# Kernel optimization log

Hardware: AMD Instinct MI355X
Metric: run time of the kernel (lower is better)

## Reference

```python
import jax, jax.numpy as jnp
import numpy as np

N, E, S = 20000, 160000, 3        # nodes, edges, message-passing steps
L, NODE_D, EDGE_D, OUT = 128, 12, 7, 3
LN_EPS = 1e-5


def _mlp(x, W0, b0, W1, b1, W2, b2):
    # Linear -> ReLU -> Linear -> ReLU -> Linear (widths: in->L->L->out)
    h = jax.nn.relu(x @ W0 + b0)
    h = jax.nn.relu(h @ W1 + b1)
    return h @ W2 + b2


def _ln(h, g, b):
    mu = jnp.mean(h, axis=-1, keepdims=True)
    var = jnp.mean((h - mu) ** 2, axis=-1, keepdims=True)
    return (h - mu) * jax.lax.rsqrt(var + LN_EPS) * g + b


def setup_inputs() -> dict:
    ks = iter(jax.random.split(jax.random.key(0), 64))
    w = lambda *s: jax.random.normal(next(ks), s, jnp.float32) * 0.05
    z = lambda *s: jnp.zeros(s, jnp.float32)
    o = lambda *s: jnp.ones(s, jnp.float32)
    inp = {
        'node_x': jax.random.normal(next(ks), (N, NODE_D), jnp.float32),
        'edge_x': jax.random.normal(next(ks), (E, EDGE_D), jnp.float32),
        'enc_n_W0': w(NODE_D, L), 'enc_n_b0': z(L), 'enc_n_W1': w(L, L), 'enc_n_b1': z(L),
        'enc_n_W2': w(L, L), 'enc_n_b2': z(L), 'enc_n_g': o(L), 'enc_n_be': z(L),
        'enc_e_W0': w(EDGE_D, L), 'enc_e_b0': z(L), 'enc_e_W1': w(L, L), 'enc_e_b1': z(L),
        'enc_e_W2': w(L, L), 'enc_e_b2': z(L), 'enc_e_g': o(L), 'enc_e_be': z(L),
        'gnb_e_W0': w(S, 3 * L, L), 'gnb_e_b0': z(S, L), 'gnb_e_W1': w(S, L, L), 'gnb_e_b1': z(S, L),
        'gnb_e_W2': w(S, L, L), 'gnb_e_b2': z(S, L), 'gnb_e_g': o(S, L), 'gnb_e_be': z(S, L),
        'gnb_n_W0': w(S, 2 * L, L), 'gnb_n_b0': z(S, L), 'gnb_n_W1': w(S, L, L), 'gnb_n_b1': z(S, L),
        'gnb_n_W2': w(S, L, L), 'gnb_n_b2': z(S, L), 'gnb_n_g': o(S, L), 'gnb_n_be': z(S, L),
        'dec_W0': w(L, L), 'dec_b0': z(L), 'dec_W1': w(L, L), 'dec_b1': z(L),
        'dec_W2': w(L, OUT), 'dec_b2': z(OUT),
        'senders': jax.random.randint(next(ks), (E,), 0, N, jnp.int32),
        'receivers': jax.random.randint(next(ks), (E,), 0, N, jnp.int32),
    }
    return inp


def reference(node_x, edge_x,
              enc_n_W0, enc_n_b0, enc_n_W1, enc_n_b1, enc_n_W2, enc_n_b2, enc_n_g, enc_n_be,
              enc_e_W0, enc_e_b0, enc_e_W1, enc_e_b1, enc_e_W2, enc_e_b2, enc_e_g, enc_e_be,
              gnb_e_W0, gnb_e_b0, gnb_e_W1, gnb_e_b1, gnb_e_W2, gnb_e_b2, gnb_e_g, gnb_e_be,
              gnb_n_W0, gnb_n_b0, gnb_n_W1, gnb_n_b1, gnb_n_W2, gnb_n_b2, gnb_n_g, gnb_n_be,
              dec_W0, dec_b0, dec_W1, dec_b1, dec_W2, dec_b2,
              senders, receivers):
    num_nodes = node_x.shape[0]
    # Encoder: MLP + LayerNorm on nodes and edges
    nf = _ln(_mlp(node_x, enc_n_W0, enc_n_b0, enc_n_W1, enc_n_b1, enc_n_W2, enc_n_b2), enc_n_g, enc_n_be)
    ef = _ln(_mlp(edge_x, enc_e_W0, enc_e_b0, enc_e_W1, enc_e_b1, enc_e_W2, enc_e_b2), enc_e_g, enc_e_be)

    def step(carry, p):
        nf, ef = carry
        (eW0, eb0, eW1, eb1, eW2, eb2, eg, ebe,
         nW0, nb0, nW1, nb1, nW2, nb2, ng, nbe) = p
        # gather sender/receiver node features -> concat with edge features -> edge MLP
        cat_e = jnp.concatenate([nf[senders], nf[receivers], ef], axis=-1)  # [E, 3L]
        new_ef = _ln(_mlp(cat_e, eW0, eb0, eW1, eb1, eW2, eb2), eg, ebe)
        # scatter-sum updated edge features to receiver nodes
        agg = jax.ops.segment_sum(new_ef, receivers, num_segments=num_nodes)  # [N, L]
        new_nf = _ln(_mlp(jnp.concatenate([nf, agg], axis=-1), nW0, nb0, nW1, nb1, nW2, nb2), ng, nbe)
        # residual connections on both nodes and edges
        return (nf + new_nf, ef + new_ef), None

    step_params = (gnb_e_W0, gnb_e_b0, gnb_e_W1, gnb_e_b1, gnb_e_W2, gnb_e_b2, gnb_e_g, gnb_e_be,
                   gnb_n_W0, gnb_n_b0, gnb_n_W1, gnb_n_b1, gnb_n_W2, gnb_n_b2, gnb_n_g, gnb_n_be)
    (nf, ef), _ = jax.lax.scan(step, (nf, ef), step_params)

    # Decoder: MLP without LayerNorm
    return _mlp(nf, dec_W0, dec_b0, dec_W1, dec_b1, dec_W2, dec_b2)
```

## Files before the change

kernel.cpp:

```cpp
#include <hip/hip_runtime.h>
#include <hip/hip_bf16.h>

#define NN 20000
#define EE 160000

typedef __attribute__((ext_vector_type(8))) short bf16x8;
typedef __attribute__((ext_vector_type(4))) float f32x4;

__device__ __forceinline__ unsigned short f2bf(float f) {
    unsigned int u = __float_as_uint(f);
    u += 0x7FFFu + ((u >> 16) & 1);
    return (unsigned short)(u >> 16);
}
__device__ __forceinline__ float bf2f(short s) {
    return __uint_as_float(((unsigned int)(unsigned short)s) << 16);
}
__device__ __forceinline__ bf16x8 pack8(float4 a, float4 b) {
    bf16x8 r;
    r[0] = (short)f2bf(a.x); r[1] = (short)f2bf(a.y);
    r[2] = (short)f2bf(a.z); r[3] = (short)f2bf(a.w);
    r[4] = (short)f2bf(b.x); r[5] = (short)f2bf(b.y);
    r[6] = (short)f2bf(b.z); r[7] = (short)f2bf(b.w);
    return r;
}

#define SH_STRIDE 136
#define SW_STRIDE 56
#define SH64 132
#define SW64 72

__device__ __forceinline__ void bar_lgkm() {
    asm volatile("s_waitcnt lgkmcnt(0)\n\ts_barrier" ::: "memory");
}

__device__ __forceinline__ void mfma_sweep_lds(f32x4 (&acc)[2][8], bf16x8 a0, bf16x8 a1,
                                               const short* sWb, int lm, int lq)
{
#pragma unroll
    for (int ct = 0; ct < 8; ++ct) {
        bf16x8 b = *(const bf16x8*)(sWb + (ct * 16 + lm) * SW_STRIDE + lq * 8);
        acc[0][ct] = __builtin_amdgcn_mfma_f32_16x16x32_bf16(a0, b, acc[0][ct], 0, 0, 0);
        acc[1][ct] = __builtin_amdgcn_mfma_f32_16x16x32_bf16(a1, b, acc[1][ct], 0, 0, 0);
    }
}

__device__ __forceinline__ void mfma_sweep64(f32x4 (&acc)[2][8], bf16x8 a0, bf16x8 a1,
                                             const short* sWb, int colOff, int lm)
{
#pragma unroll
    for (int ct = 0; ct < 8; ++ct) {
        bf16x8 b = *(const bf16x8*)(sWb + (ct * 16 + lm) * SW64 + colOff);
        acc[0][ct] = __builtin_amdgcn_mfma_f32_16x16x32_bf16(a0, b, acc[0][ct], 0, 0, 0);
        acc[1][ct] = __builtin_amdgcn_mfma_f32_16x16x32_bf16(a1, b, acc[1][ct], 0, 0, 0);
    }
}

template<int NT>
struct WStage { bf16x8 v[512 / NT]; };

template<int NT>
__device__ __forceinline__ void wload(WStage<NT>& ws, const short* __restrict__ Wt,
                                      int Kpad, int k0, int tid)
{
#pragma unroll
    for (int j = 0; j < 256 / NT; ++j) {
        int i = tid + j * NT;
        int r = i >> 1, h = i & 1;
        const short* src = Wt + (size_t)r * Kpad + k0 + h * 16;
        ws.v[2 * j]     = *(const bf16x8*)src;
        ws.v[2 * j + 1] = *(const bf16x8*)(src + 8);
    }
}
template<int NT>
__device__ __forceinline__ void wstore(const WStage<NT>& ws, short* __restrict__ sW, int tid)
{
#pragma unroll
    for (int j = 0; j < 256 / NT; ++j) {
        int i = tid + j * NT;
        int r = i >> 1, h = i & 1;
        short* dst = sW + r * SW_STRIDE + h * 16;
        *(bf16x8*)dst       = ws.v[2 * j];
        *(bf16x8*)(dst + 8) = ws.v[2 * j + 1];
    }
}

struct WStage64 { bf16x8 v[4]; };
__device__ __forceinline__ void wload64(WStage64& ws, const short* __restrict__ Wt,
                                        int Kpad, int k0, int tid)
{
#pragma unroll
    for (int j = 0; j < 4; ++j) {
        int i = tid + j * 256;
        int r = i >> 3, h = i & 7;
        ws.v[j] = *(const bf16x8*)(Wt + (size_t)r * Kpad + k0 + h * 8);
    }
}
__device__ __forceinline__ void wstore64(const WStage64& ws, short* __restrict__ sW, int tid)
{
#pragma unroll
    for (int j = 0; j < 4; ++j) {
        int i = tid + j * 256;
        int r = i >> 3, h = i & 7;
        *(bf16x8*)(sW + r * SW64 + h * 8) = ws.v[j];
    }
}

__device__ __forceinline__ void zero_acc(f32x4 (&acc)[2][8]) {
#pragma unroll
    for (int i = 0; i < 2; ++i)
#pragma unroll
        for (int j = 0; j < 8; ++j) acc[i][j] = (f32x4)(0.f);
}

__device__ __forceinline__ void park(const f32x4 (&acc)[2][8], const float* __restrict__ bias,
                                     short* __restrict__ sH, int w32, int lm, int lq)
{
#pragma unroll
    for (int ct = 0; ct < 8; ++ct) {
        float bb = bias[ct * 16 + lm];
#pragma unroll
        for (int rt = 0; rt < 2; ++rt) {
            int rbase = w32 + rt * 16 + lq * 4;
#pragma unroll
            for (int reg = 0; reg < 4; ++reg) {
                float v = fmaxf(acc[rt][ct][reg] + bb, 0.f);
                sH[(rbase + reg) * SH_STRIDE + ct * 16 + lm] = (short)f2bf(v);
            }
        }
    }
}

__device__ __forceinline__ void park64(const f32x4 (&acc)[2][8], const float* __restrict__ bias,
                                       short* __restrict__ sH, int w32, int lm, int lq)
{
#pragma unroll
    for (int ct = 0; ct < 8; ++ct) {
        float bb = bias[ct * 16 + lm];
#pragma unroll
        for (int rt = 0; rt < 2; ++rt) {
            int rbase = w32 + rt * 16 + lq * 4;
#pragma unroll
            for (int reg = 0; reg < 4; ++reg) {
                float v = fmaxf(acc[rt][ct][reg] + bb, 0.f);
                sH[(rbase + reg) * SH64 + ct * 16 + lm] = (short)f2bf(v);
            }
        }
    }
}

struct Frag {
    bf16x8 a0, a1;
    float4 f0, f1, f2, f3;
    int isF;
};

template<int MODE>
__device__ __forceinline__ void load_frag(Frag& fr, int c,
    const short* __restrict__ nfb, const float* __restrict__ aggf,
    int r0m, int r1m, const short* sH, int w32, int lm, int lq)
{
    int kq = lq * 8;
    fr.isF = 0;
    if (MODE == 0) {
        fr.a0 = *(const bf16x8*)&sH[(w32 + lm) * SH_STRIDE + c * 32 + kq];
        fr.a1 = *(const bf16x8*)&sH[(w32 + 16 + lm) * SH_STRIDE + c * 32 + kq];
    } else if (MODE == 2) {
        int seg = c >> 2, kb = (c & 3) * 32 + kq;
        if (seg == 0) {
            fr.a0 = *(const bf16x8*)(nfb + (size_t)r0m * 128 + kb);
            fr.a1 = *(const bf16x8*)(nfb + (size_t)r1m * 128 + kb);
        } else {
            const float* p0 = aggf + (size_t)r0m * 128 + kb;
            const float* p1 = aggf + (size_t)r1m * 128 + kb;
            fr.f0 = *(const float4*)p0; fr.f1 = *(const float4*)(p0 + 4);
            fr.f2 = *(const float4*)p1; fr.f3 = *(const float4*)(p1 + 4);
            fr.isF = 1;
        }
    } else {
        int kb = c * 32 + kq;
        fr.a0 = *(const bf16x8*)(nfb + (size_t)r0m * 128 + kb);
        fr.a1 = *(const bf16x8*)(nfb + (size_t)r1m * 128 + kb);
    }
}

struct Frag64 { bf16x8 a[4]; };

__device__ __forceinline__ void load_frag64(Frag64& fr, int c,
    const short* __restrict__ nfb, const short* __restrict__ efHi,
    int iS0, int iS1, int iR0, int iR1, size_t eO0, size_t eO1, int lq)
{
    int kb = (c & 1) * 64 + lq * 8;
    int seg = c >> 1;
    const short *base0, *base1;
    if (seg == 0)      { base0 = nfb + (size_t)iS0 * 128; base1 = nfb + (size_t)iS1 * 128; }
    else if (seg == 1) { base0 = nfb + (size_t)iR0 * 128; base1 = nfb + (size_t)iR1 * 128; }
    else               { base0 = efHi + eO0;              base1 = efHi + eO1; }
    fr.a[0] = *(const bf16x8*)(base0 + kb);
    fr.a[1] = *(const bf16x8*)(base1 + kb);
    fr.a[2] = *(const bf16x8*)(base0 + kb + 32);
    fr.a[3] = *(const bf16x8*)(base1 + kb + 32);
}

template<int RESID>
__global__ __launch_bounds__(256) void gnn_edge64(
    const short* __restrict__ Wt0,
    const short* __restrict__ Wt1, const short* __restrict__ Wt2,
    const float* __restrict__ b0, const float* __restrict__ b1, const float* __restrict__ b2,
    const float* __restrict__ g, const float* __restrict__ be,
    const short* __restrict__ nfb,
    short* __restrict__ efHi, short* __restrict__ efLo,
    const int* __restrict__ eList,
    const int* __restrict__ senders, const int* __restrict__ receivers,
    float* __restrict__ aggOut)
{
    __shared__ short sH[128 * SH64];
    __shared__ short sW[128 * SW64];
    __shared__ int sRcv[128], sSnd[128];
    const int tid = threadIdx.x;
    const int lane = tid & 63;
    const int w = tid >> 6;
    const int lm = lane & 15;
    const int lq = lane >> 4;
    const int w32 = w * 32;
    const int m0 = blockIdx.x * 128;

    if (tid < 128) {
        int slot = m0 + tid;
        int e = eList ? eList[slot] : slot;
        sRcv[tid] = receivers[e];
        sSnd[tid] = senders[e];
    }
    bar_lgkm();

    f32x4 acc[2][8];
    zero_acc(acc);

    const int s0 = w32 + 2 * lm, s1 = s0 + 1;
    const int iS0 = sSnd[s0], iS1 = sSnd[s1];
    const int iR0 = sRcv[s0], iR1 = sRcv[s1];
    const size_t eO0 = (size_t)(m0 + s0) * 128;
    const size_t eO1 = (size_t)(m0 + s1) * 128;

    {
        WStage64 ws, wsn;
        Frag64 cur, nxt;
        wload64(ws, Wt0, 384, 0, tid);
        load_frag64(cur, 0, nfb, efHi, iS0, iS1, iR0, iR1, eO0, eO1, lq);
#pragma unroll
        for (int c = 0; c < 6; ++c) {
            if (c + 1 < 6) {
                wload64(wsn, Wt0, 384, (c + 1) * 64, tid);
                load_frag64(nxt, c + 1, nfb, efHi, iS0, iS1, iR0, iR1, eO0, eO1, lq);
            }
            bar_lgkm();
            wstore64(ws, sW, tid);
            bar_lgkm();
            mfma_sweep64(acc, cur.a[0], cur.a[1], sW, lq * 8, lm);
            mfma_sweep64(acc, cur.a[2], cur.a[3], sW, 32 + lq * 8, lm);
            ws = wsn; cur = nxt;
        }
    }
    bar_lgkm();
    park64(acc, b0, sH, w32, lm, lq);

    zero_acc(acc);
    {
        WStage64 ws, wsn;
        wload64(ws, Wt1, 128, 0, tid);
#pragma unroll
        for (int c = 0; c < 2; ++c) {
            if (c == 0) wload64(wsn, Wt1, 128, 64, tid);
            bf16x8 a0h0 = *(const bf16x8*)&sH[(w32 + lm) * SH64 + c * 64 + lq * 8];
            bf16x8 a1h0 = *(const bf16x8*)&sH[(w32 + 16 + lm) * SH64 + c * 64 + lq * 8];
            bf16x8 a0h1 = *(const bf16x8*)&sH[(w32 + lm) * SH64 + c * 64 + 32 + lq * 8];
            bf16x8 a1h1 = *(const bf16x8*)&sH[(w32 + 16 + lm) * SH64 + c * 64 + 32 + lq * 8];
            bar_lgkm();
            wstore64(ws, sW, tid);
            bar_lgkm();
            mfma_sweep64(acc, a0h0, a1h0, sW, lq * 8, lm);
            mfma_sweep64(acc, a0h1, a1h1, sW, 32 + lq * 8, lm);
            ws = wsn;
        }
    }
    bar_lgkm();
    park64(acc, b1, sH, w32, lm, lq);

    zero_acc(acc);
    {
        WStage64 ws, wsn;
        wload64(ws, Wt2, 128, 0, tid);
#pragma unroll
        for (int c = 0; c < 2; ++c) {
            if (c == 0) wload64(wsn, Wt2, 128, 64, tid);
            bf16x8 a0h0 = *(const bf16x8*)&sH[(w32 + lm) * SH64 + c * 64 + lq * 8];
            bf16x8 a1h0 = *(const bf16x8*)&sH[(w32 + 16 + lm) * SH64 + c * 64 + lq * 8];
            bf16x8 a0h1 = *(const bf16x8*)&sH[(w32 + lm) * SH64 + c * 64 + 32 + lq * 8];
            bf16x8 a1h1 = *(const bf16x8*)&sH[(w32 + 16 + lm) * SH64 + c * 64 + 32 + lq * 8];
            bar_lgkm();
            wstore64(ws, sW, tid);
            bar_lgkm();
            mfma_sweep64(acc, a0h0, a1h0, sW, lq * 8, lm);
            mfma_sweep64(acc, a0h1, a1h1, sW, 32 + lq * 8, lm);
            ws = wsn;
        }
    }

    float g_[8], be_[8], b2_[8];
#pragma unroll
    for (int ct = 0; ct < 8; ++ct) {
        g_[ct] = g[ct * 16 + lm]; be_[ct] = be[ct * 16 + lm]; b2_[ct] = b2[ct * 16 + lm];
    }
    float run[8];
    int curRcv = -1;
#pragma unroll
    for (int j = 0; j < 8; ++j) {
        int rt = j & 1, reg = j >> 1;
        int rloc = w32 + lq * 8 + j;
        float v[8];
        float s = 0.f;
#pragma unroll
        for (int ct = 0; ct < 8; ++ct) { v[ct] = acc[rt][ct][reg] + b2_[ct]; s += v[ct]; }
        s += __shfl_xor(s, 1); s += __shfl_xor(s, 2);
        s += __shfl_xor(s, 4); s += __shfl_xor(s, 8);
        float mu = s * (1.f / 128.f);
        float q = 0.f;
#pragma unroll
        for (int ct = 0; ct < 8; ++ct) { v[ct] -= mu; q += v[ct] * v[ct]; }
        q += __shfl_xor(q, 1); q += __shfl_xor(q, 2);
        q += __shfl_xor(q, 4); q += __shfl_xor(q, 8);
        float rs = rsqrtf(q * (1.f / 128.f) + 1e-5f);
        int rcv = sRcv[rloc];
        float o[8];
#pragma unroll
        for (int ct = 0; ct < 8; ++ct) {
            o[ct] = v[ct] * rs * g_[ct] + be_[ct];
            if (RESID) {
                size_t gi = (size_t)(m0 + rloc) * 128 + ct * 16 + lm;
                float x = bf2f(efHi[gi]) + bf2f(efLo[gi]) + o[ct];
                short h = (short)f2bf(x);
                efHi[gi] = h;
                efLo[gi] = (short)f2bf(x - bf2f(h));
            }
        }
        if (rcv != curRcv) {
            if (curRcv >= 0) {
#pragma unroll
                for (int ct = 0; ct < 8; ++ct)
                    atomicAdd(aggOut + (size_t)curRcv * 128 + ct * 16 + lm, run[ct]);
            }
            curRcv = rcv;
#pragma unroll
            for (int ct = 0; ct < 8; ++ct) run[ct] = o[ct];
        } else {
#pragma unroll
            for (int ct = 0; ct < 8; ++ct) run[ct] += o[ct];
        }
    }
    if (curRcv >= 0) {
#pragma unroll
        for (int ct = 0; ct < 8; ++ct)
            atomicAdd(aggOut + (size_t)curRcv * 128 + ct * 16 + lm, run[ct]);
    }
}

template<int NW, int MODE, int PAIR>
__global__ __launch_bounds__(NW * 64) void gnn_mlp(
    const short* __restrict__ Wt0,
    const short* __restrict__ Wt1, const short* __restrict__ Wt2,
    const float* __restrict__ b0, const float* __restrict__ b1, const float* __restrict__ b2,
    const float* __restrict__ g, const float* __restrict__ be,
    const float* __restrict__ A0f, int K0,
    const short* __restrict__ nfb,
    const float* __restrict__ aggf,
    const int* __restrict__ eList,
    float* __restrict__ outF, short* __restrict__ outB, short* __restrict__ outB2,
    float* __restrict__ aggOut,
    float* __restrict__ decOut,
    int M, int resid)
{
    constexpr int KP0 = (MODE == 2) ? 256 : (MODE == 3) ? 128 : 32;
    constexpr int nC0 = KP0 / 32;
    __shared__ short sH[NW * 32 * SH_STRIDE];
    __shared__ short sW[128 * SW_STRIDE];
    const int tid = threadIdx.x;
    const int lane = tid & 63;
    const int w = tid >> 6;
    const int lm = lane & 15;
    const int lq = lane >> 4;
    const int w32 = w * 32;
    const int m0 = blockIdx.x * (NW * 32);
    constexpr int NT = NW * 64;

    f32x4 acc[2][8];
    zero_acc(acc);

    if (MODE == 0) {
#pragma unroll
        for (int i = 0; i < 16; ++i) {
            int flat = lane + i * 64;
            int r = flat >> 5, k = flat & 31;
            int row = m0 + w32 + r;
            float v = 0.f;
            if (k < K0 && row < M) {
                int src = eList ? eList[row] : row;
                v = A0f[(size_t)src * K0 + k];
            }
            sH[(w32 + r) * SH_STRIDE + k] = (short)f2bf(v);
        }
    }
    const int r0m = min(m0 + w32 + lm, M - 1);
    const int r1m = min(m0 + w32 + 16 + lm, M - 1);

    {
        WStage<NT> ws, wsn;
        Frag cur, nx1, nx2;
        wload<NT>(ws, Wt0, KP0, 0, tid);
        load_frag<MODE>(cur, 0, nfb, aggf, r0m, r1m, sH, w32, lm, lq);
        if (nC0 > 1)
            load_frag<MODE>(nx1, 1, nfb, aggf, r0m, r1m, sH, w32, lm, lq);
#pragma unroll
        for (int c = 0; c < nC0; ++c) {
            if (c + 1 < nC0)
                wload<NT>(wsn, Wt0, KP0, (c + 1) * 32, tid);
            if (c + 2 < nC0)
                load_frag<MODE>(nx2, c + 2, nfb, aggf, r0m, r1m, sH, w32, lm, lq);
            bar_lgkm();
            wstore<NT>(ws, sW, tid);
            bar_lgkm();
            bf16x8 u0, u1;
            if (cur.isF) { u0 = pack8(cur.f0, cur.f1); u1 = pack8(cur.f2, cur.f3); }
            else         { u0 = cur.a0;               u1 = cur.a1; }
            mfma_sweep_lds(acc, u0, u1, sW, lm, lq);
            ws = wsn; cur = nx1; nx1 = nx2;
        }
    }
    bar_lgkm();
    park(acc, b0, sH, w32, lm, lq);

    if (MODE == 2 && aggOut) {
        int totalF4 = NW * 32 * 32;
        for (int i = tid; i < totalF4; i += NT) {
            int r = i >> 5, c4 = i & 31;
            int row = m0 + r;
            if (row < M)
                *(float4*)(aggOut + (size_t)row * 128 + c4 * 4) = make_float4(0.f, 0.f, 0.f, 0.f);
        }
    }

    zero_acc(acc);
    {
        WStage<NT> ws, wsn;
        wload<NT>(ws, Wt1, 128, 0, tid);
#pragma unroll
        for (int c = 0; c < 4; ++c) {
            if (c + 1 < 4) wload<NT>(wsn, Wt1, 128, (c + 1) * 32, tid);
            bf16x8 a0 = *(const bf16x8*)&sH[(w32 + lm) * SH_STRIDE + c * 32 + lq * 8];
            bf16x8 a1 = *(const bf16x8*)&sH[(w32 + 16 + lm) * SH_STRIDE + c * 32 + lq * 8];
            bar_lgkm();
            wstore<NT>(ws, sW, tid);
            bar_lgkm();
            mfma_sweep_lds(acc, a0, a1, sW, lm, lq);
            ws = wsn;
        }
    }
    bar_lgkm();
    park(acc, b1, sH, w32, lm, lq);

    if (MODE == 3) {
#pragma unroll
        for (int t = 0; t < 2; ++t) {
            int idx = t * 64 + lane;
            if (idx < 96) {
                int r = idx / 3, o = idx - r * 3;
                int row = m0 + w32 + r;
                if (row < M) {
                    float s = b2[o];
#pragma unroll
                    for (int kk = 0; kk < 16; ++kk) {
                        bf16x8 h8 = *(const bf16x8*)&sH[(w32 + r) * SH_STRIDE + kk * 8];
#pragma unroll
                        for (int j = 0; j < 8; ++j)
                            s += bf2f(h8[j]) * A0f[(kk * 8 + j) * 3 + o];
                    }
                    decOut[(size_t)row * 3 + o] = s;
                }
            }
        }
        return;
    }

    zero_acc(acc);
    {
        WStage<NT> ws, wsn;
        wload<NT>(ws, Wt2, 128, 0, tid);
#pragma unroll
        for (int c = 0; c < 4; ++c) {
            if (c + 1 < 4) wload<NT>(wsn, Wt2, 128, (c + 1) * 32, tid);
            bf16x8 a0 = *(const bf16x8*)&sH[(w32 + lm) * SH_STRIDE + c * 32 + lq * 8];
            bf16x8 a1 = *(const bf16x8*)&sH[(w32 + 16 + lm) * SH_STRIDE + c * 32 + lq * 8];
            bar_lgkm();
            wstore<NT>(ws, sW, tid);
            bar_lgkm();
            mfma_sweep_lds(acc, a0, a1, sW, lm, lq);
            ws = wsn;
        }
    }

    float g_[8], be_[8], b2_[8];
#pragma unroll
    for (int ct = 0; ct < 8; ++ct) {
        g_[ct] = g[ct * 16 + lm]; be_[ct] = be[ct * 16 + lm]; b2_[ct] = b2[ct * 16 + lm];
    }
#pragma unroll
    for (int rt = 0; rt < 2; ++rt) {
#pragma unroll
        for (int reg = 0; reg < 4; ++reg) {
            int row = m0 + w32 + rt * 16 + lq * 4 + reg;
            float v[8];
            float s = 0.f;
#pragma unroll
            for (int ct = 0; ct < 8; ++ct) { v[ct] = acc[rt][ct][reg] + b2_[ct]; s += v[ct]; }
            s += __shfl_xor(s, 1); s += __shfl_xor(s, 2);
            s += __shfl_xor(s, 4); s += __shfl_xor(s, 8);
            float mu = s * (1.f / 128.f);
            float q = 0.f;
#pragma unroll
            for (int ct = 0; ct < 8; ++ct) { v[ct] -= mu; q += v[ct] * v[ct]; }
            q += __shfl_xor(q, 1); q += __shfl_xor(q, 2);
            q += __shfl_xor(q, 4); q += __shfl_xor(q, 8);
            float rs = rsqrtf(q * (1.f / 128.f) + 1e-5f);
            if (row < M) {
#pragma unroll
                for (int ct = 0; ct < 8; ++ct) {
                    float o = v[ct] * rs * g_[ct] + be_[ct];
                    size_t gi = (size_t)row * 128 + ct * 16 + lm;
                    if (PAIR) {
                        short h = (short)f2bf(o);
                        outB[gi]  = h;
                        outB2[gi] = (short)f2bf(o - bf2f(h));
                    } else {
                        if (resid) {
                            float ns = outF[gi] + o;
                            outF[gi] = ns;
                            if (outB) outB[gi] = (short)f2bf(ns);
                        } else {
                            outF[gi] = o;
                            if (outB) outB[gi] = (short)f2bf(o);
                        }
                    }
                }
            }
        }
    }
}

__global__ void zero_i(int* __restrict__ p, int n)
{
    int i = blockIdx.x * 256 + threadIdx.x;
    if (i < n) p[i] = 0;
}
__global__ void csr_count(const int* __restrict__ recv, int* __restrict__ cnt, int E)
{
    int i = blockIdx.x * 256 + threadIdx.x;
    if (i < E) atomicAdd(&cnt[recv[i]], 1);
}
__global__ __launch_bounds__(256) void csr_scan(const int* __restrict__ cnt,
                                                int* __restrict__ cursor, int N)
{
    __shared__ int ssum[257];
    const int tid = threadIdx.x;
    const int per = (N + 255) / 256;
    const int lo = tid * per, hi = min(lo + per, N);
    int s = 0;
    for (int i = lo; i < hi; ++i) s += cnt[i];
    ssum[tid] = s;
    __syncthreads();
    if (tid == 0) {
        int run = 0;
        for (int i = 0; i < 256; ++i) { int t = ssum[i]; ssum[i] = run; run += t; }
        ssum[256] = run;
    }
    __syncthreads();
    int run = ssum[tid];
    for (int i = lo; i < hi; ++i) { int c = cnt[i]; cursor[i] = run; run += c; }
}
__global__ void csr_fill(const int* __restrict__ recv, int* __restrict__ cursor,
                         int* __restrict__ eList, int E)
{
    int i = blockIdx.x * 256 + threadIdx.x;
    if (i < E) {
        int pos = atomicAdd(&cursor[recv[i]], 1);
        eList[pos] = i;
    }
}

struct WtPrep { const float* src; int K; int Kpad; int dstOff; };
struct WtPrepAll { WtPrep m[26]; };

__global__ void wt_prep_kernel(WtPrepAll all, short* __restrict__ dst)
{
    const WtPrep p = all.m[blockIdx.y];
    int total = 128 * p.Kpad;
    int idx = blockIdx.x * 256 + threadIdx.x;
    if (idx >= total) return;
    int n = idx / p.Kpad, k = idx - n * p.Kpad;
    float v = (k < p.K) ? p.src[(size_t)k * 128 + n] : 0.f;
    dst[p.dstOff + idx] = (short)f2bf(v);
}

__global__ void zero_kernel(float4* __restrict__ p, long n4)
{
    long i = (long)blockIdx.x * blockDim.x + threadIdx.x;
    if (i < n4) p[i] = make_float4(0.f, 0.f, 0.f, 0.f);
}

extern "C" void kernel_launch(void* const* d_in, const int* in_sizes, int n_in,
                              void* d_out, int out_size, void* d_ws, size_t ws_size,
                              hipStream_t stream)
{
    const float* node_x   = (const float*)d_in[0];
    const float* edge_x   = (const float*)d_in[1];
    const float* enc_n_W0 = (const float*)d_in[2];
    const float* enc_n_b0 = (const float*)d_in[3];
    const float* enc_n_W1 = (const float*)d_in[4];
    const float* enc_n_b1 = (const float*)d_in[5];
    const float* enc_n_W2 = (const float*)d_in[6];
    const float* enc_n_b2 = (const float*)d_in[7];
    const float* enc_n_g  = (const float*)d_in[8];
    const float* enc_n_be = (const float*)d_in[9];
    const float* enc_e_W0 = (const float*)d_in[10];
    const float* enc_e_b0 = (const float*)d_in[11];
    const float* enc_e_W1 = (const float*)d_in[12];
    const float* enc_e_b1 = (const float*)d_in[13];
    const float* enc_e_W2 = (const float*)d_in[14];
    const float* enc_e_b2 = (const float*)d_in[15];
    const float* enc_e_g  = (const float*)d_in[16];
    const float* enc_e_be = (const float*)d_in[17];
    const float* gnb_e_W0 = (const float*)d_in[18];
    const float* gnb_e_b0 = (const float*)d_in[19];
    const float* gnb_e_W1 = (const float*)d_in[20];
    const float* gnb_e_b1 = (const float*)d_in[21];
    const float* gnb_e_W2 = (const float*)d_in[22];
    const float* gnb_e_b2 = (const float*)d_in[23];
    const float* gnb_e_g  = (const float*)d_in[24];
    const float* gnb_e_be = (const float*)d_in[25];
    const float* gnb_n_W0 = (const float*)d_in[26];
    const float* gnb_n_b0 = (const float*)d_in[27];
    const float* gnb_n_W1 = (const float*)d_in[28];
    const float* gnb_n_b1 = (const float*)d_in[29];
    const float* gnb_n_W2 = (const float*)d_in[30];
    const float* gnb_n_b2 = (const float*)d_in[31];
    const float* gnb_n_g  = (const float*)d_in[32];
    const float* gnb_n_be = (const float*)d_in[33];
    const float* dec_W0   = (const float*)d_in[34];
    const float* dec_b0   = (const float*)d_in[35];
    const float* dec_W1   = (const float*)d_in[36];
    const float* dec_b1   = (const float*)d_in[37];
    const float* dec_W2   = (const float*)d_in[38];
    const float* dec_b2   = (const float*)d_in[39];
    const int*   senders  = (const int*)d_in[40];
    const int*   receivers= (const int*)d_in[41];
    float* out = (float*)d_out;

    const int N = NN, E = EE;
    const int WT_TOTAL = (32 + 128 + 128 + 32 + 128 + 128 + 3 * (384 + 128 + 128 + 256 + 128 + 128)
                          + 128 + 128) * 128;

    float* nf   = (float*)d_ws;
    float* agg  = nf + (size_t)N * 128;
    short* efHi = (short*)(agg + (size_t)N * 128);
    short* efLo = efHi + (size_t)E * 128;
    short* nfbf = efLo + (size_t)E * 128;
    short* wt   = nfbf + (size_t)N * 128;
    int*   eList = (int*)(wt + WT_TOTAL);
    size_t need_sorted = (size_t)((char*)(eList + E) - (char*)d_ws);
    int* cnt    = (int*)agg;
    int* cursor = cnt + N;

    const bool useSorted = (ws_size >= need_sorted);
    const int* eL = useSorted ? eList : nullptr;

    WtPrepAll tbl;
    int nMat = 0, off = 0;
    int o_encn[3], o_ence[3], o_ge0[3], o_ge1[3], o_ge2[3], o_gn0[3], o_gn1[3], o_gn2[3], o_dec[2];
    auto add = [&](const float* src, int K, int Kpad) {
        tbl.m[nMat].src = src; tbl.m[nMat].K = K; tbl.m[nMat].Kpad = Kpad;
        tbl.m[nMat].dstOff = off;
        int r = off; off += 128 * Kpad; ++nMat; return r;
    };
    o_encn[0] = add(enc_n_W0, 12, 32);
    o_encn[1] = add(enc_n_W1, 128, 128);
    o_encn[2] = add(enc_n_W2, 128, 128);
    o_ence[0] = add(enc_e_W0, 7, 32);
    o_ence[1] = add(enc_e_W1, 128, 128);
    o_ence[2] = add(enc_e_W2, 128, 128);
    for (int s = 0; s < 3; ++s) {
        o_ge0[s] = add(gnb_e_W0 + (size_t)s * 384 * 128, 384, 384);
        o_ge1[s] = add(gnb_e_W1 + (size_t)s * 128 * 128, 128, 128);
        o_ge2[s] = add(gnb_e_W2 + (size_t)s * 128 * 128, 128, 128);
        o_gn0[s] = add(gnb_n_W0 + (size_t)s * 256 * 128, 256, 256);
        o_gn1[s] = add(gnb_n_W1 + (size_t)s * 128 * 128, 128, 128);
        o_gn2[s] = add(gnb_n_W2 + (size_t)s * 128 * 128, 128, 128);
    }
    o_dec[0] = add(dec_W0, 128, 128);
    o_dec[1] = add(dec_W1, 128, 128);

    wt_prep_kernel<<<dim3(192, 26), 256, 0, stream>>>(tbl, wt);

    if (useSorted) {
        zero_i<<<dim3((N + 255) / 256), 256, 0, stream>>>(cnt, N);
        csr_count<<<dim3((E + 255) / 256), 256, 0, stream>>>(receivers, cnt, E);
        csr_scan<<<dim3(1), 256, 0, stream>>>(cnt, cursor, N);
        csr_fill<<<dim3((E + 255) / 256), 256, 0, stream>>>(receivers, cursor, eList, E);
    }
    zero_kernel<<<dim3((N * 32 + 255) / 256), 256, 0, stream>>>((float4*)agg, (long)N * 32);

    const dim3 gE(E / 128);
    const dim3 gN2((N + 63) / 64);

    gnn_mlp<2, 0, 0><<<gN2, 128, 0, stream>>>(wt + o_encn[0], wt + o_encn[1], wt + o_encn[2],
        enc_n_b0, enc_n_b1, enc_n_b2, enc_n_g, enc_n_be,
        node_x, 12, nullptr, nullptr, nullptr,
        nf, nfbf, nullptr, nullptr, nullptr, N, 0);
    gnn_mlp<4, 0, 1><<<gE, 256, 0, stream>>>(wt + o_ence[0], wt + o_ence[1], wt + o_ence[2],
        enc_e_b0, enc_e_b1, enc_e_b2, enc_e_g, enc_e_be,
        edge_x, 7, nullptr, nullptr, eL,
        nullptr, efHi, efLo, nullptr, nullptr, E, 0);

    for (int s = 0; s < 3; ++s) {
        const float* eb0 = gnb_e_b0 + (size_t)s * 128;
        const float* eb1 = gnb_e_b1 + (size_t)s * 128;
        const float* eb2 = gnb_e_b2 + (size_t)s * 128;
        const float* eg  = gnb_e_g  + (size_t)s * 128;
        const float* ebe = gnb_e_be + (size_t)s * 128;
        const float* nb0 = gnb_n_b0 + (size_t)s * 128;
        const float* nb1 = gnb_n_b1 + (size_t)s * 128;
        const float* nb2 = gnb_n_b2 + (size_t)s * 128;
        const float* ng  = gnb_n_g  + (size_t)s * 128;
        const float* nbe = gnb_n_be + (size_t)s * 128;

        if (s < 2) {
            gnn_edge64<1><<<gE, 256, 0, stream>>>(wt + o_ge0[s], wt + o_ge1[s], wt + o_ge2[s],
                eb0, eb1, eb2, eg, ebe,
                nfbf, efHi, efLo, eL, senders, receivers, agg);
        } else {
            gnn_edge64<0><<<gE, 256, 0, stream>>>(wt + o_ge0[s], wt + o_ge1[s], wt + o_ge2[s],
                eb0, eb1, eb2, eg, ebe,
                nfbf, efHi, efLo, eL, senders, receivers, agg);
        }
        gnn_mlp<2, 2, 0><<<gN2, 128, 0, stream>>>(wt + o_gn0[s], wt + o_gn1[s], wt + o_gn2[s],
            nb0, nb1, nb2, ng, nbe,
            nullptr, 0, nfbf, agg, nullptr,
            nf, nfbf, nullptr, agg, nullptr, N, 1);
    }

    gnn_mlp<2, 3, 0><<<gN2, 128, 0, stream>>>(wt + o_dec[0], wt + o_dec[1], nullptr,
        dec_b0, dec_b1, dec_b2, nullptr, nullptr,
        dec_W2, 0, nfbf, nullptr, nullptr,
        nullptr, nullptr, nullptr, nullptr, out, N, 0);
}
```

Measured before the change: 608.7 us.

## Read MFMA weight fragments directly from global memory instead of LDS staging

```diff
diff --git a/kernel.cpp b/kernel.cpp
--- a/kernel.cpp
+++ b/kernel.cpp
@@ -25,83 +25,17 @@
 }
 
 #define SH_STRIDE 136
-#define SW_STRIDE 56
 #define SH64 132
-#define SW64 72
-
-__device__ __forceinline__ void bar_lgkm() {
-    asm volatile("s_waitcnt lgkmcnt(0)\n\ts_barrier" ::: "memory");
-}
-
-__device__ __forceinline__ void mfma_sweep_lds(f32x4 (&acc)[2][8], bf16x8 a0, bf16x8 a1,
-                                               const short* sWb, int lm, int lq)
+
+template<int KPAD>
+__device__ __forceinline__ void mfma_sweepG(f32x4 (&acc)[2][8], bf16x8 a0, bf16x8 a1,
+                                            const short* __restrict__ Bp)
 {
 #pragma unroll
     for (int ct = 0; ct < 8; ++ct) {
-        bf16x8 b = *(const bf16x8*)(sWb + (ct * 16 + lm) * SW_STRIDE + lq * 8);
+        bf16x8 b = *(const bf16x8*)(Bp + (size_t)ct * 16 * KPAD);
         acc[0][ct] = __builtin_amdgcn_mfma_f32_16x16x32_bf16(a0, b, acc[0][ct], 0, 0, 0);
         acc[1][ct] = __builtin_amdgcn_mfma_f32_16x16x32_bf16(a1, b, acc[1][ct], 0, 0, 0);
-    }
-}
-
-__device__ __forceinline__ void mfma_sweep64(f32x4 (&acc)[2][8], bf16x8 a0, bf16x8 a1,
-                                             const short* sWb, int colOff, int lm)
-{
-#pragma unroll
-    for (int ct = 0; ct < 8; ++ct) {
-        bf16x8 b = *(const bf16x8*)(sWb + (ct * 16 + lm) * SW64 + colOff);
-        acc[0][ct] = __builtin_amdgcn_mfma_f32_16x16x32_bf16(a0, b, acc[0][ct], 0, 0, 0);
-        acc[1][ct] = __builtin_amdgcn_mfma_f32_16x16x32_bf16(a1, b, acc[1][ct], 0, 0, 0);
-    }
-}
-
-template<int NT>
-struct WStage { bf16x8 v[512 / NT]; };
-
-template<int NT>
-__device__ __forceinline__ void wload(WStage<NT>& ws, const short* __restrict__ Wt,
-                                      int Kpad, int k0, int tid)
-{
-#pragma unroll
-    for (int j = 0; j < 256 / NT; ++j) {
-        int i = tid + j * NT;
-        int r = i >> 1, h = i & 1;
-        const short* src = Wt + (size_t)r * Kpad + k0 + h * 16;
-        ws.v[2 * j]     = *(const bf16x8*)src;
-        ws.v[2 * j + 1] = *(const bf16x8*)(src + 8);
-    }
-}
-template<int NT>
-__device__ __forceinline__ void wstore(const WStage<NT>& ws, short* __restrict__ sW, int tid)
-{
-#pragma unroll
-    for (int j = 0; j < 256 / NT; ++j) {
-        int i = tid + j * NT;
-        int r = i >> 1, h = i & 1;
-        short* dst = sW + r * SW_STRIDE + h * 16;
-        *(bf16x8*)dst       = ws.v[2 * j];
-        *(bf16x8*)(dst + 8) = ws.v[2 * j + 1];
-    }
-}
-
-struct WStage64 { bf16x8 v[4]; };
-__device__ __forceinline__ void wload64(WStage64& ws, const short* __restrict__ Wt,
-                                        int Kpad, int k0, int tid)
-{
-#pragma unroll
-    for (int j = 0; j < 4; ++j) {
-        int i = tid + j * 256;
-        int r = i >> 3, h = i & 7;
-        ws.v[j] = *(const bf16x8*)(Wt + (size_t)r * Kpad + k0 + h * 8);
-    }
-}
-__device__ __forceinline__ void wstore64(const WStage64& ws, short* __restrict__ sW, int tid)
-{
-#pragma unroll
-    for (int j = 0; j < 4; ++j) {
-        int i = tid + j * 256;
-        int r = i >> 3, h = i & 7;
-        *(bf16x8*)(sW + r * SW64 + h * 8) = ws.v[j];
     }
 }
 
@@ -202,7 +136,7 @@
 }
 
 template<int RESID>
-__global__ __launch_bounds__(256) void gnn_edge64(
+__global__ __launch_bounds__(256, 4) void gnn_edge64(
     const short* __restrict__ Wt0,
     const short* __restrict__ Wt1, const short* __restrict__ Wt2,
     const float* __restrict__ b0, const float* __restrict__ b1, const float* __restrict__ b2,
@@ -214,7 +148,6 @@
     float* __restrict__ aggOut)
 {
     __shared__ short sH[128 * SH64];
-    __shared__ short sW[128 * SW64];
     __shared__ int sRcv[128], sSnd[128];
     const int tid = threadIdx.x;
     const int lane = tid & 63;
@@ -224,13 +157,12 @@
     const int w32 = w * 32;
     const int m0 = blockIdx.x * 128;
 
-    if (tid < 128) {
-        int slot = m0 + tid;
+    if (lane < 32) {
+        int slot = m0 + w32 + lane;
         int e = eList ? eList[slot] : slot;
-        sRcv[tid] = receivers[e];
-        sSnd[tid] = senders[e];
-    }
-    bar_lgkm();
+        sRcv[w32 + lane] = receivers[e];
+        sSnd[w32 + lane] = senders[e];
+    }
 
     f32x4 acc[2][8];
     zero_acc(acc);
@@ -241,68 +173,45 @@
     const size_t eO0 = (size_t)(m0 + s0) * 128;
     const size_t eO1 = (size_t)(m0 + s1) * 128;
 
+    const short* B0 = Wt0 + (size_t)lm * 384 + lq * 8;
+    const short* B1 = Wt1 + (size_t)lm * 128 + lq * 8;
+    const short* B2 = Wt2 + (size_t)lm * 128 + lq * 8;
+
     {
-        WStage64 ws, wsn;
         Frag64 cur, nxt;
-        wload64(ws, Wt0, 384, 0, tid);
         load_frag64(cur, 0, nfb, efHi, iS0, iS1, iR0, iR1, eO0, eO1, lq);
 #pragma unroll
         for (int c = 0; c < 6; ++c) {
-            if (c + 1 < 6) {
-                wload64(wsn, Wt0, 384, (c + 1) * 64, tid);
+            if (c + 1 < 6)
                 load_frag64(nxt, c + 1, nfb, efHi, iS0, iS1, iR0, iR1, eO0, eO1, lq);
-            }
-            bar_lgkm();
-            wstore64(ws, sW, tid);
-            bar_lgkm();
-            mfma_sweep64(acc, cur.a[0], cur.a[1], sW, lq * 8, lm);
-            mfma_sweep64(acc, cur.a[2], cur.a[3], sW, 32 + lq * 8, lm);
-            ws = wsn; cur = nxt;
-        }
-    }
-    bar_lgkm();
+            mfma_sweepG<384>(acc, cur.a[0], cur.a[1], B0 + c * 64);
+            mfma_sweepG<384>(acc, cur.a[2], cur.a[3], B0 + c * 64 + 32);
+            cur = nxt;
+        }
+    }
     park64(acc, b0, sH, w32, lm, lq);
 
     zero_acc(acc);
-    {
-        WStage64 ws, wsn;
-        wload64(ws, Wt1, 128, 0, tid);
-#pragma unroll
-        for (int c = 0; c < 2; ++c) {
-            if (c == 0) wload64(wsn, Wt1, 128, 64, tid);
-            bf16x8 a0h0 = *(const bf16x8*)&sH[(w32 + lm) * SH64 + c * 64 + lq * 8];
-            bf16x8 a1h0 = *(const bf16x8*)&sH[(w32 + 16 + lm) * SH64 + c * 64 + lq * 8];
-            bf16x8 a0h1 = *(const bf16x8*)&sH[(w32 + lm) * SH64 + c * 64 + 32 + lq * 8];
-            bf16x8 a1h1 = *(const bf16x8*)&sH[(w32 + 16 + lm) * SH64 + c * 64 + 32 + lq * 8];
-            bar_lgkm();
-            wstore64(ws, sW, tid);
-            bar_lgkm();
-            mfma_sweep64(acc, a0h0, a1h0, sW, lq * 8, lm);
-            mfma_sweep64(acc, a0h1, a1h1, sW, 32 + lq * 8, lm);
-            ws = wsn;
-        }
-    }
-    bar_lgkm();
+#pragma unroll
+    for (int c = 0; c < 2; ++c) {
+        bf16x8 a0h0 = *(const bf16x8*)&sH[(w32 + lm) * SH64 + c * 64 + lq * 8];
+        bf16x8 a1h0 = *(const bf16x8*)&sH[(w32 + 16 + lm) * SH64 + c * 64 + lq * 8];
+        bf16x8 a0h1 = *(const bf16x8*)&sH[(w32 + lm) * SH64 + c * 64 + 32 + lq * 8];
+        bf16x8 a1h1 = *(const bf16x8*)&sH[(w32 + 16 + lm) * SH64 + c * 64 + 32 + lq * 8];
+        mfma_sweepG<128>(acc, a0h0, a1h0, B1 + c * 64);
+        mfma_sweepG<128>(acc, a0h1, a1h1, B1 + c * 64 + 32);
+    }
     park64(acc, b1, sH, w32, lm, lq);
 
     zero_acc(acc);
-    {
-        WStage64 ws, wsn;
-        wload64(ws, Wt2, 128, 0, tid);
-#pragma unroll
-        for (int c = 0; c < 2; ++c) {
-            if (c == 0) wload64(wsn, Wt2, 128, 64, tid);
-            bf16x8 a0h0 = *(const bf16x8*)&sH[(w32 + lm) * SH64 + c * 64 + lq * 8];
-            bf16x8 a1h0 = *(const bf16x8*)&sH[(w32 + 16 + lm) * SH64 + c * 64 + lq * 8];
-            bf16x8 a0h1 = *(const bf16x8*)&sH[(w32 + lm) * SH64 + c * 64 + 32 + lq * 8];
-            bf16x8 a1h1 = *(const bf16x8*)&sH[(w32 + 16 + lm) * SH64 + c * 64 + 32 + lq * 8];
-            bar_lgkm();
-            wstore64(ws, sW, tid);
-            bar_lgkm();
-            mfma_sweep64(acc, a0h0, a1h0, sW, lq * 8, lm);
-            mfma_sweep64(acc, a0h1, a1h1, sW, 32 + lq * 8, lm);
-            ws = wsn;
-        }
+#pragma unroll
+    for (int c = 0; c < 2; ++c) {
+        bf16x8 a0h0 = *(const bf16x8*)&sH[(w32 + lm) * SH64 + c * 64 + lq * 8];
+        bf16x8 a1h0 = *(const bf16x8*)&sH[(w32 + 16 + lm) * SH64 + c * 64 + lq * 8];
+        bf16x8 a0h1 = *(const bf16x8*)&sH[(w32 + lm) * SH64 + c * 64 + 32 + lq * 8];
+        bf16x8 a1h1 = *(const bf16x8*)&sH[(w32 + 16 + lm) * SH64 + c * 64 + 32 + lq * 8];
+        mfma_sweepG<128>(acc, a0h0, a1h0, B2 + c * 64);
+        mfma_sweepG<128>(acc, a0h1, a1h1, B2 + c * 64 + 32);
     }
 
     float g_[8], be_[8], b2_[8];
@@ -381,7 +290,6 @@
     constexpr int KP0 = (MODE == 2) ? 256 : (MODE == 3) ? 128 : 32;
     constexpr int nC0 = KP0 / 32;
     __shared__ short sH[NW * 32 * SH_STRIDE];
-    __shared__ short sW[128 * SW_STRIDE];
     const int tid = threadIdx.x;
     const int lane = tid & 63;
     const int w = tid >> 6;
@@ -411,33 +319,27 @@
     const int r0m = min(m0 + w32 + lm, M - 1);
     const int r1m = min(m0 + w32 + 16 + lm, M - 1);
 
+    const short* B0 = Wt0 + (size_t)lm * KP0 + lq * 8;
+    const short* B1 = Wt1 + (size_t)lm * 128 + lq * 8;
+
     {
-        WStage<NT> ws, wsn;
-        Frag cur, nx1, nx2;
-        wload<NT>(ws, Wt0, KP0, 0, tid);
+        Frag cur, nxt;
         load_frag<MODE>(cur, 0, nfb, aggf, r0m, r1m, sH, w32, lm, lq);
-        if (nC0 > 1)
-            load_frag<MODE>(nx1, 1, nfb, aggf, r0m, r1m, sH, w32, lm, lq);
 #pragma unroll
         for (int c = 0; c < nC0; ++c) {
             if (c + 1 < nC0)
-                wload<NT>(wsn, Wt0, KP0, (c + 1) * 32, tid);
-            if (c + 2 < nC0)
-                load_frag<MODE>(nx2, c + 2, nfb, aggf, r0m, r1m, sH, w32, lm, lq);
-            bar_lgkm();
-            wstore<NT>(ws, sW, tid);
-            bar_lgkm();
+                load_frag<MODE>(nxt, c + 1, nfb, aggf, r0m, r1m, sH, w32, lm, lq);
             bf16x8 u0, u1;
             if (cur.isF) { u0 = pack8(cur.f0, cur.f1); u1 = pack8(cur.f2, cur.f3); }
             else         { u0 = cur.a0;               u1 = cur.a1; }
-            mfma_sweep_lds(acc, u0, u1, sW, lm, lq);
-            ws = wsn; cur = nx1; nx1 = nx2;
-        }
-    }
-    bar_lgkm();
+            mfma_sweepG<KP0>(acc, u0, u1, B0 + c * 32);
+            cur = nxt;
+        }
+    }
     park(acc, b0, sH, w32, lm, lq);
 
     if (MODE == 2 && aggOut) {
+        __syncthreads();
         int totalF4 = NW * 32 * 32;
         for (int i = tid; i < totalF4; i += NT) {
             int r = i >> 5, c4 = i & 31;
@@ -448,22 +350,12 @@
     }
 
     zero_acc(acc);
-    {
-        WStage<NT> ws, wsn;
-        wload<NT>(ws, Wt1, 128, 0, tid);
-#pragma unroll
-        for (int c = 0; c < 4; ++c) {
-            if (c + 1 < 4) wload<NT>(wsn, Wt1, 128, (c + 1) * 32, tid);
-            bf16x8 a0 = *(const bf16x8*)&sH[(w32 + lm) * SH_STRIDE + c * 32 + lq * 8];
-            bf16x8 a1 = *(const bf16x8*)&sH[(w32 + 16 + lm) * SH_STRIDE + c * 32 + lq * 8];
-            bar_lgkm();
-            wstore<NT>(ws, sW, tid);
-            bar_lgkm();
-            mfma_sweep_lds(acc, a0, a1, sW, lm, lq);
-            ws = wsn;
-        }
-    }
-    bar_lgkm();
+#pragma unroll
+    for (int c = 0; c < 4; ++c) {
+        bf16x8 a0 = *(const bf16x8*)&sH[(w32 + lm) * SH_STRIDE + c * 32 + lq * 8];
+        bf16x8 a1 = *(const bf16x8*)&sH[(w32 + 16 + lm) * SH_STRIDE + c * 32 + lq * 8];
+        mfma_sweepG<128>(acc, a0, a1, B1 + c * 32);
+    }
     park(acc, b1, sH, w32, lm, lq);
 
     if (MODE == 3) {
@@ -489,21 +381,13 @@
         return;
     }
 
+    const short* B2 = Wt2 + (size_t)lm * 128 + lq * 8;
     zero_acc(acc);
-    {
-        WStage<NT> ws, wsn;
-        wload<NT>(ws, Wt2, 128, 0, tid);
-#pragma unroll
-        for (int c = 0; c < 4; ++c) {
-            if (c + 1 < 4) wload<NT>(wsn, Wt2, 128, (c + 1) * 32, tid);
-            bf16x8 a0 = *(const bf16x8*)&sH[(w32 + lm) * SH_STRIDE + c * 32 + lq * 8];
-            bf16x8 a1 = *(const bf16x8*)&sH[(w32 + 16 + lm) * SH_STRIDE + c * 32 + lq * 8];
-            bar_lgkm();
-            wstore<NT>(ws, sW, tid);
-            bar_lgkm();
-            mfma_sweep_lds(acc, a0, a1, sW, lm, lq);
-            ws = wsn;
-        }
+#pragma unroll
+    for (int c = 0; c < 4; ++c) {
+        bf16x8 a0 = *(const bf16x8*)&sH[(w32 + lm) * SH_STRIDE + c * 32 + lq * 8];
+        bf16x8 a1 = *(const bf16x8*)&sH[(w32 + 16 + lm) * SH_STRIDE + c * 32 + lq * 8];
+        mfma_sweepG<128>(acc, a0, a1, B2 + c * 32);
     }
 
     float g_[8], be_[8], b2_[8];
```

Measured after the change: 972.3 us. 1.6x slower.

## Add node-MLP kernel with 32-row tiles and column-split waves

Applied to the files above, without the earlier changes.

```diff
diff --git a/kernel.cpp b/kernel.cpp
--- a/kernel.cpp
+++ b/kernel.cpp
@@ -55,6 +55,17 @@
     }
 }
 
+__device__ __forceinline__ void mfma_sweepNS(f32x4 (&acc)[4], bf16x8 a,
+                                             const short* sWb, int ch, int colOff, int lm)
+{
+#pragma unroll
+    for (int i = 0; i < 4; ++i) {
+        int ct = ch * 4 + i;
+        bf16x8 b = *(const bf16x8*)(sWb + (ct * 16 + lm) * SW64 + colOff);
+        acc[i] = __builtin_amdgcn_mfma_f32_16x16x32_bf16(a, b, acc[i], 0, 0, 0);
+    }
+}
+
 template<int NT>
 struct WStage { bf16x8 v[512 / NT]; };
 
@@ -126,6 +137,21 @@
                 float v = fmaxf(acc[rt][ct][reg] + bb, 0.f);
                 sH[(rbase + reg) * SH_STRIDE + ct * 16 + lm] = (short)f2bf(v);
             }
+        }
+    }
+}
+
+__device__ __forceinline__ void parkNS(const f32x4 (&acc)[4], const float* __restrict__ bias,
+                                       short* __restrict__ sH, int g16, int ch, int lm, int lq)
+{
+#pragma unroll
+    for (int i = 0; i < 4; ++i) {
+        int ct = ch * 4 + i;
+        float bb = bias[ct * 16 + lm];
+#pragma unroll
+        for (int reg = 0; reg < 4; ++reg) {
+            float v = fmaxf(acc[i][reg] + bb, 0.f);
+            sH[(g16 + lq * 4 + reg) * SH_STRIDE + ct * 16 + lm] = (short)f2bf(v);
         }
     }
 }
@@ -183,6 +209,23 @@
     }
 }
 
+template<int MODE>
+__device__ __forceinline__ void load_fragNS(Frag& fr, int c,
+    const short* __restrict__ nfb, const float* __restrict__ aggf, int r0m, int lq)
+{
+    fr.isF = 0;
+    if (MODE == 2 && c >= 2) {
+        const float* p = aggf + (size_t)r0m * 128 + (c - 2) * 64 + lq * 8;
+        fr.f0 = *(const float4*)p;        fr.f1 = *(const float4*)(p + 4);
+        fr.f2 = *(const float4*)(p + 32); fr.f3 = *(const float4*)(p + 36);
+        fr.isF = 1;
+    } else {
+        const short* p = nfb + (size_t)r0m * 128 + c * 64 + lq * 8;
+        fr.a0 = *(const bf16x8*)p;
+        fr.a1 = *(const bf16x8*)(p + 32);
+    }
+}
+
 struct Frag64 { bf16x8 a[4]; };
 
 __device__ __forceinline__ void load_frag64(Frag64& fr, int c,
@@ -437,16 +480,6 @@
     bar_lgkm();
     park(acc, b0, sH, w32, lm, lq);
 
-    if (MODE == 2 && aggOut) {
-        int totalF4 = NW * 32 * 32;
-        for (int i = tid; i < totalF4; i += NT) {
-            int r = i >> 5, c4 = i & 31;
-            int row = m0 + r;
-            if (row < M)
-                *(float4*)(aggOut + (size_t)row * 128 + c4 * 4) = make_float4(0.f, 0.f, 0.f, 0.f);
-        }
-    }
-
     zero_acc(acc);
     {
         WStage<NT> ws, wsn;
@@ -465,29 +498,6 @@
     }
     bar_lgkm();
     park(acc, b1, sH, w32, lm, lq);
-
-    if (MODE == 3) {
-#pragma unroll
-        for (int t = 0; t < 2; ++t) {
-            int idx = t * 64 + lane;
-            if (idx < 96) {
-                int r = idx / 3, o = idx - r * 3;
-                int row = m0 + w32 + r;
-                if (row < M) {
-                    float s = b2[o];
-#pragma unroll
-                    for (int kk = 0; kk < 16; ++kk) {
-                        bf16x8 h8 = *(const bf16x8*)&sH[(w32 + r) * SH_STRIDE + kk * 8];
-#pragma unroll
-                        for (int j = 0; j < 8; ++j)
-                            s += bf2f(h8[j]) * A0f[(kk * 8 + j) * 3 + o];
-                    }
-                    decOut[(size_t)row * 3 + o] = s;
-                }
-            }
-        }
-        return;
-    }
 
     zero_acc(acc);
     {
@@ -548,6 +558,213 @@
                             if (outB) outB[gi] = (short)f2bf(o);
                         }
                     }
+                }
+            }
+        }
+    }
+}
+
+template<int MODE>
+__global__ __launch_bounds__(256) void gnn_mlpNS(
+    const short* __restrict__ Wt0,
+    const short* __restrict__ Wt1, const short* __restrict__ Wt2,
+    const float* __restrict__ b0, const float* __restrict__ b1, const float* __restrict__ b2,
+    const float* __restrict__ g, const float* __restrict__ be,
+    const float* __restrict__ A0f, int K0,
+    const short* __restrict__ nfb,
+    const float* __restrict__ aggf,
+    float* __restrict__ outF, short* __restrict__ outB,
+    float* __restrict__ aggOut,
+    float* __restrict__ decOut,
+    int M, int resid)
+{
+    __shared__ short sH[32 * SH_STRIDE];
+    __shared__ short sW[128 * SW64];
+    __shared__ float sX[2][32];
+    __shared__ float sY[2][32];
+    const int tid = threadIdx.x;
+    const int lane = tid & 63;
+    const int w = tid >> 6;
+    const int gidx = w >> 1;
+    const int ch = w & 1;
+    const int lm = lane & 15;
+    const int lq = lane >> 4;
+    const int g16 = gidx * 16;
+    const int m0 = blockIdx.x * 32;
+    const int r0m = min(m0 + g16 + lm, M - 1);
+
+    f32x4 acc[4];
+#pragma unroll
+    for (int i = 0; i < 4; ++i) acc[i] = (f32x4)(0.f);
+
+    if (MODE == 0) {
+#pragma unroll
+        for (int i = 0; i < 4; ++i) {
+            int flat = tid + i * 256;
+            int r = flat >> 5, k = flat & 31;
+            int row = m0 + r;
+            float v = (k < K0 && row < M) ? A0f[(size_t)row * K0 + k] : 0.f;
+            sH[r * SH_STRIDE + k] = (short)f2bf(v);
+        }
+        {
+            const short* src = Wt0 + (size_t)(tid >> 1) * 32 + (tid & 1) * 16;
+            bf16x8 w0 = *(const bf16x8*)src;
+            bf16x8 w1 = *(const bf16x8*)(src + 8);
+            bar_lgkm();
+            short* dst = sW + (tid >> 1) * SW64 + (tid & 1) * 16;
+            *(bf16x8*)dst       = w0;
+            *(bf16x8*)(dst + 8) = w1;
+            bar_lgkm();
+        }
+        bf16x8 a0 = *(const bf16x8*)&sH[(g16 + lm) * SH_STRIDE + lq * 8];
+        mfma_sweepNS(acc, a0, sW, ch, lq * 8, lm);
+    } else {
+        constexpr int KP0 = (MODE == 2) ? 256 : 128;
+        constexpr int nC0 = KP0 / 64;
+        WStage64 ws, wsn;
+        Frag cur, nxt;
+        wload64(ws, Wt0, KP0, 0, tid);
+        load_fragNS<MODE>(cur, 0, nfb, aggf, r0m, lq);
+#pragma unroll
+        for (int c = 0; c < nC0; ++c) {
+            if (c + 1 < nC0) {
+                wload64(wsn, Wt0, KP0, (c + 1) * 64, tid);
+                load_fragNS<MODE>(nxt, c + 1, nfb, aggf, r0m, lq);
+            }
+            bar_lgkm();
+            wstore64(ws, sW, tid);
+            bar_lgkm();
+            bf16x8 u0, u1;
+            if (cur.isF) { u0 = pack8(cur.f0, cur.f1); u1 = pack8(cur.f2, cur.f3); }
+            else         { u0 = cur.a0;                u1 = cur.a1; }
+            mfma_sweepNS(acc, u0, sW, ch, lq * 8, lm);
+            mfma_sweepNS(acc, u1, sW, ch, 32 + lq * 8, lm);
+            ws = wsn; cur = nxt;
+        }
+    }
+    bar_lgkm();
+    parkNS(acc, b0, sH, g16, ch, lm, lq);
+    bar_lgkm();
+
+    if (MODE == 2 && aggOut) {
+#pragma unroll
+        for (int i = 0; i < 4; ++i) {
+            int idx = tid + i * 256;
+            int r = idx >> 5, c4 = idx & 31;
+            int row = m0 + r;
+            if (row < M)
+                *(float4*)(aggOut + (size_t)row * 128 + c4 * 4) = make_float4(0.f, 0.f, 0.f, 0.f);
+        }
+    }
+
+#pragma unroll
+    for (int i = 0; i < 4; ++i) acc[i] = (f32x4)(0.f);
+    {
+        WStage64 ws, wsn;
+        wload64(ws, Wt1, 128, 0, tid);
+#pragma unroll
+        for (int c = 0; c < 2; ++c) {
+            if (c == 0) wload64(wsn, Wt1, 128, 64, tid);
+            bf16x8 a0 = *(const bf16x8*)&sH[(g16 + lm) * SH_STRIDE + c * 64 + lq * 8];
+            bf16x8 a1 = *(const bf16x8*)&sH[(g16 + lm) * SH_STRIDE + c * 64 + 32 + lq * 8];
+            bar_lgkm();
+            wstore64(ws, sW, tid);
+            bar_lgkm();
+            mfma_sweepNS(acc, a0, sW, ch, lq * 8, lm);
+            mfma_sweepNS(acc, a1, sW, ch, 32 + lq * 8, lm);
+            ws = wsn;
+        }
+    }
+    bar_lgkm();
+    parkNS(acc, b1, sH, g16, ch, lm, lq);
+    bar_lgkm();
+
+    if (MODE == 3) {
+        if (tid < 96) {
+            int r = tid / 3, o = tid - r * 3;
+            int row = m0 + r;
+            if (row < M) {
+                float s = b2[o];
+#pragma unroll
+                for (int kk = 0; kk < 16; ++kk) {
+                    bf16x8 h8 = *(const bf16x8*)&sH[r * SH_STRIDE + kk * 8];
+#pragma unroll
+                    for (int j = 0; j < 8; ++j)
+                        s += bf2f(h8[j]) * A0f[(kk * 8 + j) * 3 + o];
+                }
+                decOut[(size_t)row * 3 + o] = s;
+            }
+        }
+        return;
+    }
+
+#pragma unroll
+    for (int i = 0; i < 4; ++i) acc[i] = (f32x4)(0.f);
+    {
+        WStage64 ws, wsn;
+        wload64(ws, Wt2, 128, 0, tid);
+#pragma unroll
+        for (int c = 0; c < 2; ++c) {
+            if (c == 0) wload64(wsn, Wt2, 128, 64, tid);
+            bf16x8 a0 = *(const bf16x8*)&sH[(g16 + lm) * SH_STRIDE + c * 64 + lq * 8];
+            bf16x8 a1 = *(const bf16x8*)&sH[(g16 + lm) * SH_STRIDE + c * 64 + 32 + lq * 8];
+            bar_lgkm();
+            wstore64(ws, sW, tid);
+            bar_lgkm();
+            mfma_sweepNS(acc, a0, sW, ch, lq * 8, lm);
+            mfma_sweepNS(acc, a1, sW, ch, 32 + lq * 8, lm);
+            ws = wsn;
+        }
+    }
+
+    float g_[4], be_[4], b2_[4];
+#pragma unroll
+    for (int i = 0; i < 4; ++i) {
+        int ct = ch * 4 + i;
+        g_[i] = g[ct * 16 + lm]; be_[i] = be[ct * 16 + lm]; b2_[i] = b2[ct * 16 + lm];
+    }
+    float v[4][4], mu[4], rs_[4];
+#pragma unroll
+    for (int reg = 0; reg < 4; ++reg) {
+        float s = 0.f;
+#pragma unroll
+        for (int i = 0; i < 4; ++i) { v[i][reg] = acc[i][reg] + b2_[i]; s += v[i][reg]; }
+        s += __shfl_xor(s, 1); s += __shfl_xor(s, 2);
+        s += __shfl_xor(s, 4); s += __shfl_xor(s, 8);
+        if (lm == 0) sX[ch][g16 + lq * 4 + reg] = s;
+    }
+    bar_lgkm();
+#pragma unroll
+    for (int reg = 0; reg < 4; ++reg)
+        mu[reg] = (sX[0][g16 + lq * 4 + reg] + sX[1][g16 + lq * 4 + reg]) * (1.f / 128.f);
+#pragma unroll
+    for (int reg = 0; reg < 4; ++reg) {
+        float q = 0.f;
+#pragma unroll
+        for (int i = 0; i < 4; ++i) { v[i][reg] -= mu[reg]; q += v[i][reg] * v[i][reg]; }
+        q += __shfl_xor(q, 1); q += __shfl_xor(q, 2);
+        q += __shfl_xor(q, 4); q += __shfl_xor(q, 8);
+        if (lm == 0) sY[ch][g16 + lq * 4 + reg] = q;
+    }
+    bar_lgkm();
+#pragma unroll
+    for (int reg = 0; reg < 4; ++reg)
+        rs_[reg] = rsqrtf((sY[0][g16 + lq * 4 + reg] + sY[1][g16 + lq * 4 + reg]) * (1.f / 128.f) + 1e-5f);
+#pragma unroll
+    for (int reg = 0; reg < 4; ++reg) {
+        int row = m0 + g16 + lq * 4 + reg;
+        if (row < M) {
+#pragma unroll
+            for (int i = 0; i < 4; ++i) {
+                float o = v[i][reg] * rs_[reg] * g_[i] + be_[i];
+                size_t gi = (size_t)row * 128 + (size_t)(ch * 4 + i) * 16 + lm;
+                if (resid) {
+                    float ns = outF[gi] + o;
+                    outF[gi] = ns;
+                    if (outB) outB[gi] = (short)f2bf(ns);
+                } else {
+                    outF[gi] = o;
+                    if (outB) outB[gi] = (short)f2bf(o);
                 }
             }
         }
@@ -716,12 +933,12 @@
     zero_kernel<<<dim3((N * 32 + 255) / 256), 256, 0, stream>>>((float4*)agg, (long)N * 32);
 
     const dim3 gE(E / 128);
-    const dim3 gN2((N + 63) / 64);
-
-    gnn_mlp<2, 0, 0><<<gN2, 128, 0, stream>>>(wt + o_encn[0], wt + o_encn[1], wt + o_encn[2],
+    const dim3 gNS(N / 32);
+
+    gnn_mlpNS<0><<<gNS, 256, 0, stream>>>(wt + o_encn[0], wt + o_encn[1], wt + o_encn[2],
         enc_n_b0, enc_n_b1, enc_n_b2, enc_n_g, enc_n_be,
-        node_x, 12, nullptr, nullptr, nullptr,
-        nf, nfbf, nullptr, nullptr, nullptr, N, 0);
+        node_x, 12, nullptr, nullptr,
+        nf, nfbf, nullptr, nullptr, N, 0);
     gnn_mlp<4, 0, 1><<<gE, 256, 0, stream>>>(wt + o_ence[0], wt + o_ence[1], wt + o_ence[2],
         enc_e_b0, enc_e_b1, enc_e_b2, enc_e_g, enc_e_be,
         edge_x, 7, nullptr, nullptr, eL,
@@ -748,14 +965,14 @@
                 eb0, eb1, eb2, eg, ebe,
                 nfbf, efHi, efLo, eL, senders, receivers, agg);
         }
-        gnn_mlp<2, 2, 0><<<gN2, 128, 0, stream>>>(wt + o_gn0[s], wt + o_gn1[s], wt + o_gn2[s],
+        gnn_mlpNS<2><<<gNS, 256, 0, stream>>>(wt + o_gn0[s], wt + o_gn1[s], wt + o_gn2[s],
             nb0, nb1, nb2, ng, nbe,
-            nullptr, 0, nfbf, agg, nullptr,
-            nf, nfbf, nullptr, agg, nullptr, N, 1);
-    }
-
-    gnn_mlp<2, 3, 0><<<gN2, 128, 0, stream>>>(wt + o_dec[0], wt + o_dec[1], nullptr,
+            nullptr, 0, nfbf, agg,
+            nf, nfbf, agg, nullptr, N, 1);
+    }
+
+    gnn_mlpNS<3><<<gNS, 256, 0, stream>>>(wt + o_dec[0], wt + o_dec[1], nullptr,
         dec_b0, dec_b1, dec_b2, nullptr, nullptr,
-        dec_W2, 0, nfbf, nullptr, nullptr,
-        nullptr, nullptr, nullptr, nullptr, out, N, 0);
-}
+        dec_W2, 0, nfbf, nullptr,
+        nullptr, nullptr, nullptr, out, N, 0);
+}
```

Result: faster. 563.8 us (-7.4%).
